# Kernel tuning notes

Measured on AMD Instinct MI355X. Metric: run time of the kernel, lower is better.

## Reference

```python
import jax, jax.numpy as jnp
import numpy as np

EMBED_DIM = 1024
NUM_HEADS = 16
HEAD_DIM = EMBED_DIM // NUM_HEADS
B, S = 4, 2048


def setup_inputs() -> dict:
    key = jax.random.key(0)
    k1, k2, k3, k4, k5 = jax.random.split(key, 5)
    x = jax.random.normal(k1, (B, S, EMBED_DIM), dtype=jnp.float32)
    # torch nn.Linear params: W [out, in], b [out]; init scale ~ 1/sqrt(in)
    s = 1.0 / np.sqrt(EMBED_DIM)
    qkv_w = jax.random.uniform(k2, (3 * EMBED_DIM, EMBED_DIM), jnp.float32, -s, s)
    qkv_b = jax.random.uniform(k3, (3 * EMBED_DIM,), jnp.float32, -s, s)
    out_w = jax.random.uniform(k4, (EMBED_DIM, EMBED_DIM), jnp.float32, -s, s)
    out_b = jax.random.uniform(k5, (EMBED_DIM,), jnp.float32, -s, s)
    return {"x": x, "qkv_w": qkv_w, "qkv_b": qkv_b, "out_w": out_w, "out_b": out_b}


def reference(x, qkv_w, qkv_b, out_w, out_b):
    b, s, e = x.shape
    # qkv: [B,S,3E]
    qkv = x @ qkv_w.T + qkv_b
    # Faithful to source: reshape to [B,S,H,3*hd] then transpose -> [B,H,S,3*hd]
    qkv = qkv.reshape(b, s, NUM_HEADS, 3 * HEAD_DIM).transpose(0, 2, 1, 3)
    q, k, v = jnp.split(qkv, 3, axis=-1)  # each [B,H,S,hd]
    q = q / np.sqrt(HEAD_DIM).astype(np.float32)
    scores = jnp.einsum('bhqd,bhkd->bhqk', q, k)  # [B,H,S,S]
    attn = jax.nn.softmax(scores, axis=-1)
    out = jnp.einsum('bhqk,bhkd->bhqd', attn, v)  # [B,H,S,hd]
    out = out.transpose(0, 2, 1, 3).reshape(b, s, e)
    return out @ out_w.T + out_b
```

## Files before the change

kernel.cpp:

```cpp
#include <hip/hip_runtime.h>

#define EMBED   1024
#define THREE_E 3072
#define NHEAD   16
#define HDIM    64
#define BATCH   4
#define SEQ     2048
#define MTOK    (BATCH * SEQ)
#define QKW     2048

typedef __attribute__((ext_vector_type(8))) _Float16 half8;
typedef __attribute__((ext_vector_type(4))) _Float16 half4;
typedef __attribute__((ext_vector_type(4))) float    f32x4;

#define QSCALE 0.18033688011112042f

__device__ inline f32x4 mfma16(half8 a, half8 b, f32x4 c) {
    return __builtin_amdgcn_mfma_f32_16x16x32_f16(a, b, c, 0, 0, 0);
}
__device__ inline f32x4 mfma16k16(half4 a, half4 b, f32x4 c) {
    return __builtin_amdgcn_mfma_f32_16x16x16f16(a, b, c, 0, 0, 0);
}

__device__ inline float exp2x(float x) {
    float r;
    asm("v_exp_f32 %0, %1" : "=v"(r) : "v"(x));
    return r;
}

__device__ inline void gld16(const void* g, void* l) {
    __builtin_amdgcn_global_load_lds(
        (const __attribute__((address_space(1))) unsigned*)g,
        (__attribute__((address_space(3))) unsigned*)l, 16, 0, 0);
}

__global__ __launch_bounds__(256) void tohi3_kernel(
    const float* __restrict__ x,  _Float16* __restrict__ xo,
    const float* __restrict__ w1, _Float16* __restrict__ w1o,
    const float* __restrict__ w2, _Float16* __restrict__ w2o)
{
    const int bid = blockIdx.x;
    const float* src; _Float16* dst; int base;
    if (bid < 8192)             { src = x;  dst = xo;  base = bid * 1024; }
    else if (bid < 8192 + 3072) { src = w1; dst = w1o; base = (bid - 8192) * 1024; }
    else                        { src = w2; dst = w2o; base = (bid - 11264) * 1024; }
    const int i = base + (threadIdx.x << 2);
    const float4 v = *(const float4*)(src + i);
    half4 h;
    h[0] = (_Float16)v.x; h[1] = (_Float16)v.y;
    h[2] = (_Float16)v.z; h[3] = (_Float16)v.w;
    *(half4*)(dst + i) = h;
}

template<int OMODE>
__global__ __launch_bounds__(512, 2) void gemm_big(
    const _Float16* __restrict__ Ahi,
    const _Float16* __restrict__ Bhi,
    const float*  __restrict__ bias,
    float* __restrict__ Cf,
    _Float16* __restrict__ QKhi,
    _Float16* __restrict__ Vthi,
    int N, int K)
{
    __shared__ __align__(16) _Float16 sA[3][8][2][64][8];
    __shared__ __align__(16) _Float16 sB[3][16][2][64][8];

    const int tid  = threadIdx.x;
    const int w    = tid >> 6;
    const int lane = tid & 63;
    const int quad = lane >> 4;
    const int c    = lane & 15;
    const int wr   = w >> 2, wc = w & 3;

    const int gx   = gridDim.x;
    const int nwg  = gx * gridDim.y;
    const int lin0 = blockIdx.y * gx + blockIdx.x;
    const int wg   = (lin0 & 7) * (nwg >> 3) + (lin0 >> 3);
    const int m0   = (wg / gx) << 7;
    const int n0   = (wg % gx) << 8;

    f32x4 acc[4][4];
#pragma unroll
    for (int i = 0; i < 4; ++i)
#pragma unroll
        for (int j = 0; j < 4; ++j) acc[i][j] = (f32x4){0.f, 0.f, 0.f, 0.f};

    const int rg0 = w >> 1, ksb = w & 1;
    const size_t sK64 = (size_t)64 * K;
    const _Float16* ap = Ahi + (size_t)(m0 + rg0 * 16 + c) * K + ksb * 32 + quad * 8;
    const _Float16* bp = Bhi + (size_t)(n0 + rg0 * 16 + c) * K + ksb * 32 + quad * 8;

    auto stage_p0 = [&](int sl) {
        gld16(ap,            &sA[sl][rg0][ksb][0][0]);
        gld16(ap + sK64,     &sA[sl][4 + rg0][ksb][0][0]);
        gld16(bp,            &sB[sl][rg0][ksb][0][0]);
    };
    auto stage_p1 = [&](int sl) {
        gld16(bp + sK64,     &sB[sl][4 + rg0][ksb][0][0]);
        gld16(bp + 2 * sK64, &sB[sl][8 + rg0][ksb][0][0]);
        gld16(bp + 3 * sK64, &sB[sl][12 + rg0][ksb][0][0]);
        ap += 64; bp += 64;
    };

    stage_p0(0); stage_p1(0);
    stage_p0(1); stage_p1(1);

    const int NT = K >> 6;
    int slot = 0;
    for (int t = 0; t < NT; ++t) {
        if (t + 1 < NT) { asm volatile("s_waitcnt vmcnt(6)" ::: "memory"); }
        else            { asm volatile("s_waitcnt vmcnt(0)" ::: "memory"); }
        __builtin_amdgcn_s_barrier();

        const bool pre = (t + 2) < NT;
        int ns = slot + 2; if (ns >= 3) ns -= 3;

        half8 aH[4][2], bH[4][2];
#pragma unroll
        for (int fr = 0; fr < 4; ++fr)
#pragma unroll
            for (int ks = 0; ks < 2; ++ks)
                aH[fr][ks] = *(const half8*)&sA[slot][wr * 4 + fr][ks][lane][0];
#pragma unroll
        for (int fc = 0; fc < 2; ++fc)
#pragma unroll
            for (int ks = 0; ks < 2; ++ks)
                bH[fc][ks] = *(const half8*)&sB[slot][wc * 4 + fc][ks][lane][0];
        if (pre) stage_p0(ns);
        __builtin_amdgcn_s_setprio(1);
#pragma unroll
        for (int fr = 0; fr < 4; ++fr)
#pragma unroll
            for (int fc = 0; fc < 2; ++fc)
#pragma unroll
                for (int ks = 0; ks < 2; ++ks)
                    acc[fr][fc] = mfma16(aH[fr][ks], bH[fc][ks], acc[fr][fc]);
        __builtin_amdgcn_s_setprio(0);
        __builtin_amdgcn_s_barrier();

#pragma unroll
        for (int fc = 2; fc < 4; ++fc)
#pragma unroll
            for (int ks = 0; ks < 2; ++ks)
                bH[fc][ks] = *(const half8*)&sB[slot][wc * 4 + fc][ks][lane][0];
        if (pre) stage_p1(ns);
        __builtin_amdgcn_s_setprio(1);
#pragma unroll
        for (int fr = 0; fr < 4; ++fr)
#pragma unroll
            for (int fc = 2; fc < 4; ++fc)
#pragma unroll
                for (int ks = 0; ks < 2; ++ks)
                    acc[fr][fc] = mfma16(aH[fr][ks], bH[fc][ks], acc[fr][fc]);
        __builtin_amdgcn_s_setprio(0);

        slot = (slot == 2) ? 0 : slot + 1;
    }

#pragma unroll
    for (int fc = 0; fc < 4; ++fc) {
        const int n  = n0 + wc * 64 + fc * 16 + c;
        const float bb = bias[n];
        const int h  = n / 192;
        const int rem = n - h * 192;
#pragma unroll
        for (int fr = 0; fr < 4; ++fr) {
            const int mb = m0 + wr * 64 + fr * 16 + (quad << 2);
            if constexpr (OMODE == 0) {
#pragma unroll
                for (int r = 0; r < 4; ++r)
                    Cf[(size_t)(mb + r) * N + n] = acc[fr][fc][r] + bb;
            } else {
                if (rem < 128) {
                    const size_t col = h * 128 + rem;
                    const float scale = (rem < 64) ? QSCALE : 1.0f;
#pragma unroll
                    for (int r = 0; r < 4; ++r)
                        QKhi[(size_t)(mb + r) * QKW + col] =
                            (_Float16)((acc[fr][fc][r] + bb) * scale);
                } else {
                    const int d = rem - 128;
                    const int b = mb >> 11;
                    const int s = mb & 2047;
                    half4 h4;
#pragma unroll
                    for (int r = 0; r < 4; ++r)
                        h4[r] = (_Float16)(acc[fr][fc][r] + bb);
                    const size_t off = ((size_t)(h * 64 + d) * BATCH + b) * SEQ + s;
                    *(half4*)(Vthi + off) = h4;
                }
            }
        }
    }
}

__global__ __launch_bounds__(256, 4) void attn_mfma(
    const _Float16* __restrict__ qkhi,
    const _Float16* __restrict__ vthi,
    _Float16* __restrict__ attnf)
{
    __shared__ __align__(16) _Float16 Kf[2][8][512];
    __shared__ __align__(16) _Float16 Vf[2][8][512];

    const int tid  = threadIdx.x;
    const int w    = tid >> 6;
    const int lane = tid & 63;
    const int quad = lane >> 4;
    const int c    = lane & 15;

    const int lin = blockIdx.x;
    const int g   = lin & 7;
    const int s   = lin >> 3;
    const int bh  = g * 8 + (s >> 4);
    const int qt  = s & 15;
    const int b   = bh >> 4, h = bh & 15;
    const int q0  = qt * 128;

    const size_t bSEQ  = (size_t)b * SEQ;
    const int    qcol  = h * 128;
    const int    kcol  = h * 128 + 64;
    const size_t vbase = ((size_t)(h * 64) * BATCH + b) * SEQ;

    half8 qh[2][2];
#pragma unroll
    for (int t = 0; t < 2; ++t) {
        const size_t row = (bSEQ + q0 + w * 32 + t * 16 + c) * QKW;
#pragma unroll
        for (int ks = 0; ks < 2; ++ks)
            qh[t][ks] = *(const half8*)(qkhi + row + qcol + ks * 32 + quad * 8);
    }

    f32x4 lacc[2];
    f32x4 oacc[4][2];
#pragma unroll
    for (int t = 0; t < 2; ++t) {
        lacc[t] = (f32x4){0.f, 0.f, 0.f, 0.f};
#pragma unroll
        for (int v = 0; v < 4; ++v) oacc[v][t] = (f32x4){0.f, 0.f, 0.f, 0.f};
    }

    const half4 one4 = {(_Float16)1.f, (_Float16)1.f, (_Float16)1.f, (_Float16)1.f};

    const int ku0 = w >> 1,       kks0 = w & 1;
    const int ku1 = (4 + w) >> 1, kks1 = (4 + w) & 1;
    const _Float16* kp0 = qkhi + (bSEQ + ku0 * 16 + c) * QKW + kcol + kks0 * 32 + quad * 8;
    const _Float16* kp1 = qkhi + (bSEQ + ku1 * 16 + c) * QKW + kcol + kks1 * 32 + quad * 8;
    const int lswz = lane ^ ((((lane >> 3) & 1) << 1) | (((lane >> 4) & 1) << 2));
    const int qs   = lswz >> 4, cs = lswz & 15;
    const _Float16* vp0 = vthi + vbase + (size_t)(ku0 * 16 + cs) * (BATCH * SEQ) + kks0 * 32 + qs * 8;
    const _Float16* vp1 = vthi + vbase + (size_t)(ku1 * 16 + cs) * (BATCH * SEQ) + kks1 * 32 + qs * 8;

    auto stageKV = [&](int bfs) {
        gld16(kp0, &Kf[bfs][w][0]);
        gld16(kp1, &Kf[bfs][4 + w][0]);
        gld16(vp0, &Vf[bfs][w][0]);
        gld16(vp1, &Vf[bfs][4 + w][0]);
        kp0 += 64 * QKW; kp1 += 64 * QKW; vp0 += 64; vp1 += 64;
    };

    stageKV(0);
    int bf = 0;

    for (int kt = 0; kt < SEQ / 64; ++kt) {
        __syncthreads();
        if (kt + 1 < SEQ / 64) stageKV(bf ^ 1);

        f32x4 sacc[2][4];
        __builtin_amdgcn_s_setprio(1);
#pragma unroll
        for (int u = 0; u < 4; ++u) {
            const half8 kh0 = *(const half8*)&Kf[bf][(u << 1) + 0][lane << 3];
            const half8 kh1 = *(const half8*)&Kf[bf][(u << 1) + 1][lane << 3];
#pragma unroll
            for (int t = 0; t < 2; ++t) {
                f32x4 a = (f32x4){0.f, 0.f, 0.f, 0.f};
                a = mfma16(kh0, qh[t][0], a);
                a = mfma16(kh1, qh[t][1], a);
                sacc[t][u] = a;
            }
        }
        __builtin_amdgcn_s_setprio(0);

        half4 pk[2][4];
#pragma unroll
        for (int t = 0; t < 2; ++t)
#pragma unroll
            for (int u = 0; u < 4; ++u) {
                const float p0 = exp2x(sacc[t][u][0]);
                const float p1 = exp2x(sacc[t][u][1]);
                const float p2 = exp2x(sacc[t][u][2]);
                const float p3 = exp2x(sacc[t][u][3]);
                const auto lo = __builtin_amdgcn_cvt_pkrtz(p0, p1);
                const auto hi = __builtin_amdgcn_cvt_pkrtz(p2, p3);
                half4 pp;
                pp[0] = (_Float16)lo[0]; pp[1] = (_Float16)lo[1];
                pp[2] = (_Float16)hi[0]; pp[3] = (_Float16)hi[1];
                pk[t][u] = pp;
            }

        half4 va[4][4];
#pragma unroll
        for (int v = 0; v < 4; ++v)
#pragma unroll
            for (int u = 0; u < 4; ++u) {
                const int qp   = ((u & 1) << 1) + (quad >> 1);
                int elem = ((qp << 4) + c) * 8 + ((quad & 1) << 2);
                elem ^= (((c >> 3) & 1) << 4) ^ ((qp & 1) << 5);
                va[v][u] = *(const half4*)&Vf[bf][(v << 1) + (u >> 1)][elem];
            }

        __builtin_amdgcn_s_setprio(1);
#pragma unroll
        for (int t = 0; t < 2; ++t) {
#pragma unroll
            for (int v = 0; v < 4; ++v) {
                f32x4 a = oacc[v][t];
#pragma unroll
                for (int u = 0; u < 4; ++u)
                    a = mfma16k16(va[v][u], pk[t][u], a);
                oacc[v][t] = a;
            }
            f32x4 l = lacc[t];
#pragma unroll
            for (int u = 0; u < 4; ++u)
                l = mfma16k16(one4, pk[t][u], l);
            lacc[t] = l;
        }
        __builtin_amdgcn_s_setprio(0);

        bf ^= 1;
    }

#pragma unroll
    for (int t = 0; t < 2; ++t) {
        const float inv = 1.0f / lacc[t][0];
        const int tok = q0 + w * 32 + t * 16 + c;
#pragma unroll
        for (int v = 0; v < 4; ++v) {
            half4 o;
#pragma unroll
            for (int r = 0; r < 4; ++r) o[r] = (_Float16)(oacc[v][t][r] * inv);
            *(half4*)&attnf[(bSEQ + tok) * EMBED + h * HDIM + v * 16 + (quad << 2)] = o;
        }
    }
}

extern "C" void kernel_launch(void* const* d_in, const int* in_sizes, int n_in,
                              void* d_out, int out_size, void* d_ws, size_t ws_size,
                              hipStream_t stream)
{
    const float* x     = (const float*)d_in[0];
    const float* qkv_w = (const float*)d_in[1];
    const float* qkv_b = (const float*)d_in[2];
    const float* out_w = (const float*)d_in[3];
    const float* out_b = (const float*)d_in[4];

    _Float16* qkhi  = (_Float16*)d_ws;
    _Float16* vthi  = qkhi  + (size_t)MTOK * QKW;
    _Float16* w1hi  = vthi  + (size_t)NHEAD * HDIM * BATCH * SEQ;
    _Float16* w2hi  = w1hi  + (size_t)THREE_E * EMBED;
    _Float16* attnf = w2hi  + (size_t)EMBED * EMBED;

    _Float16* xhi = (_Float16*)d_out;

    tohi3_kernel<<<dim3(12288), 256, 0, stream>>>(x, xhi, qkv_w, w1hi, out_w, w2hi);

    gemm_big<1><<<dim3(THREE_E / 256, MTOK / 128), 512, 0, stream>>>(
        xhi, w1hi, qkv_b, nullptr, qkhi, vthi, THREE_E, EMBED);

    attn_mfma<<<dim3(1024), 256, 0, stream>>>(qkhi, vthi, attnf);

    gemm_big<0><<<dim3(EMBED / 256, MTOK / 128), 512, 0, stream>>>(
        attnf, w2hi, out_b, (float*)d_out, nullptr, nullptr, EMBED, EMBED);
}
```

Baseline: 295.6 us.

## Use K=32 MFMA for PV product and compute row sums with VALU

The P·V product now packs pairs of 16-wide key blocks into half8 operands so it can use the 16x16x32 MFMA, halving the MFMA instruction count for that stage. The row-sum accumulation no longer uses extra MFMAs against a ones vector. Each lane instead adds its exponentials in fp32 registers, and the per-row totals are reduced with two cross-lane shuffles at the end. This trades MFMA issue slots for extra VALU adds and register repacking. The K ordering of P and V must still match between operands, and the row sum is now taken in fp32 rather than from the fp16-rounded values.

```diff
diff --git a/kernel.cpp b/kernel.cpp
--- a/kernel.cpp
+++ b/kernel.cpp
@@ -9,23 +9,24 @@
 #define MTOK    (BATCH * SEQ)
 #define QKW     2048
 
-typedef __attribute__((ext_vector_type(8))) _Float16 half8;
-typedef __attribute__((ext_vector_type(4))) _Float16 half4;
-typedef __attribute__((ext_vector_type(4))) float    f32x4;
+typedef __attribute__((ext_vector_type(8)))  _Float16 half8;
+typedef __attribute__((ext_vector_type(4)))  _Float16 half4;
+typedef __attribute__((ext_vector_type(4)))  float    f32x4;
+typedef __attribute__((ext_vector_type(4)))  unsigned uint4v;
 
 #define QSCALE 0.18033688011112042f
 
 __device__ inline f32x4 mfma16(half8 a, half8 b, f32x4 c) {
     return __builtin_amdgcn_mfma_f32_16x16x32_f16(a, b, c, 0, 0, 0);
-}
-__device__ inline f32x4 mfma16k16(half4 a, half4 b, f32x4 c) {
-    return __builtin_amdgcn_mfma_f32_16x16x16f16(a, b, c, 0, 0, 0);
 }
 
 __device__ inline float exp2x(float x) {
     float r;
     asm("v_exp_f32 %0, %1" : "=v"(r) : "v"(x));
     return r;
+}
+__device__ inline unsigned pk2(float a, float b) {
+    return __builtin_bit_cast(unsigned, __builtin_amdgcn_cvt_pkrtz(a, b));
 }
 
 __device__ inline void gld16(const void* g, void* l) {
@@ -230,16 +231,12 @@
             qh[t][ks] = *(const half8*)(qkhi + row + qcol + ks * 32 + quad * 8);
     }
 
-    f32x4 lacc[2];
+    float lrun[2] = {0.f, 0.f};
     f32x4 oacc[4][2];
 #pragma unroll
-    for (int t = 0; t < 2; ++t) {
-        lacc[t] = (f32x4){0.f, 0.f, 0.f, 0.f};
+    for (int t = 0; t < 2; ++t)
 #pragma unroll
         for (int v = 0; v < 4; ++v) oacc[v][t] = (f32x4){0.f, 0.f, 0.f, 0.f};
-    }
-
-    const half4 one4 = {(_Float16)1.f, (_Float16)1.f, (_Float16)1.f, (_Float16)1.f};
 
     const int ku0 = w >> 1,       kks0 = w & 1;
     const int ku1 = (4 + w) >> 1, kks1 = (4 + w) & 1;
@@ -281,51 +278,60 @@
         }
         __builtin_amdgcn_s_setprio(0);
 
-        half4 pk[2][4];
+        half8 pb[2][2];
+#pragma unroll
+        for (int t = 0; t < 2; ++t) {
+            float rs = 0.f;
+#pragma unroll
+            for (int gp = 0; gp < 2; ++gp) {
+                uint4v wd;
+#pragma unroll
+                for (int hf = 0; hf < 2; ++hf) {
+                    const int u = 2 * gp + hf;
+                    const float p0 = exp2x(sacc[t][u][0]);
+                    const float p1 = exp2x(sacc[t][u][1]);
+                    const float p2 = exp2x(sacc[t][u][2]);
+                    const float p3 = exp2x(sacc[t][u][3]);
+                    rs += (p0 + p1) + (p2 + p3);
+                    if (hf == 0) { wd.x = pk2(p0, p1); wd.y = pk2(p2, p3); }
+                    else         { wd.z = pk2(p0, p1); wd.w = pk2(p2, p3); }
+                }
+                pb[t][gp] = __builtin_bit_cast(half8, wd);
+            }
+            lrun[t] += rs;
+        }
+
+        half8 vb[4][2];
+        {
+            const int qp0 = quad >> 1;
+            const int qp1 = 2 + (quad >> 1);
+            int e0 = ((qp0 << 4) + c) * 8 + ((quad & 1) << 2);
+            int e1 = ((qp1 << 4) + c) * 8 + ((quad & 1) << 2);
+            e0 ^= (((c >> 3) & 1) << 4) ^ ((qp0 & 1) << 5);
+            e1 ^= (((c >> 3) & 1) << 4) ^ ((qp1 & 1) << 5);
+#pragma unroll
+            for (int v = 0; v < 4; ++v)
+#pragma unroll
+                for (int gp = 0; gp < 2; ++gp) {
+                    const half4 a0 = *(const half4*)&Vf[bf][(v << 1) + gp][e0];
+                    const half4 a1 = *(const half4*)&Vf[bf][(v << 1) + gp][e1];
+                    half8 vv;
+#pragma unroll
+                    for (int i = 0; i < 4; ++i) { vv[i] = a0[i]; vv[4 + i] = a1[i]; }
+                    vb[v][gp] = vv;
+                }
+        }
+
+        __builtin_amdgcn_s_setprio(1);
 #pragma unroll
         for (int t = 0; t < 2; ++t)
-#pragma unroll
-            for (int u = 0; u < 4; ++u) {
-                const float p0 = exp2x(sacc[t][u][0]);
-                const float p1 = exp2x(sacc[t][u][1]);
-                const float p2 = exp2x(sacc[t][u][2]);
-                const float p3 = exp2x(sacc[t][u][3]);
-                const auto lo = __builtin_amdgcn_cvt_pkrtz(p0, p1);
-                const auto hi = __builtin_amdgcn_cvt_pkrtz(p2, p3);
-                half4 pp;
-                pp[0] = (_Float16)lo[0]; pp[1] = (_Float16)lo[1];
-                pp[2] = (_Float16)hi[0]; pp[3] = (_Float16)hi[1];
-                pk[t][u] = pp;
-            }
-
-        half4 va[4][4];
-#pragma unroll
-        for (int v = 0; v < 4; ++v)
-#pragma unroll
-            for (int u = 0; u < 4; ++u) {
-                const int qp   = ((u & 1) << 1) + (quad >> 1);
-                int elem = ((qp << 4) + c) * 8 + ((quad & 1) << 2);
-                elem ^= (((c >> 3) & 1) << 4) ^ ((qp & 1) << 5);
-                va[v][u] = *(const half4*)&Vf[bf][(v << 1) + (u >> 1)][elem];
-            }
-
-        __builtin_amdgcn_s_setprio(1);
-#pragma unroll
-        for (int t = 0; t < 2; ++t) {
 #pragma unroll
             for (int v = 0; v < 4; ++v) {
                 f32x4 a = oacc[v][t];
-#pragma unroll
-                for (int u = 0; u < 4; ++u)
-                    a = mfma16k16(va[v][u], pk[t][u], a);
+                a = mfma16(vb[v][0], pb[t][0], a);
+                a = mfma16(vb[v][1], pb[t][1], a);
                 oacc[v][t] = a;
             }
-            f32x4 l = lacc[t];
-#pragma unroll
-            for (int u = 0; u < 4; ++u)
-                l = mfma16k16(one4, pk[t][u], l);
-            lacc[t] = l;
-        }
         __builtin_amdgcn_s_setprio(0);
 
         bf ^= 1;
@@ -333,7 +339,10 @@
 
 #pragma unroll
     for (int t = 0; t < 2; ++t) {
-        const float inv = 1.0f / lacc[t][0];
+        float lr = lrun[t];
+        lr += __shfl_xor(lr, 16);
+        lr += __shfl_xor(lr, 32);
+        const float inv = 1.0f / lr;
         const int tok = q0 + w * 32 + t * 16 + c;
 #pragma unroll
         for (int v = 0; v < 4; ++v) {
```

After: 289.5 us. -2.1%, faster.
